# Performance work log

Measured on AMD Instinct MI355X. Metric: run time of the kernel, lower is better.

Reference implementation:

```python
import jax, jax.numpy as jnp
import numpy as np

N_HEADS = 16

def setup_inputs() -> dict:
    key = jax.random.key(0)
    k1, k2, k3 = jax.random.split(key, 3)
    B, S, D = 4, 2048, 1024
    x = jax.random.normal(k1, (B, S, D), dtype=jnp.float32)
    w_in = jax.random.normal(k2, (D, 3 * D), dtype=jnp.float32) * (1.0 / np.sqrt(D))
    b_in = jnp.zeros((3 * D,), dtype=jnp.float32)
    w_out = jax.random.normal(k3, (D, D), dtype=jnp.float32) * (1.0 / np.sqrt(D))
    b_out = jnp.zeros((D,), dtype=jnp.float32)
    return {"x": x, "w_in": w_in, "b_in": b_in, "w_out": w_out, "b_out": b_out}

def reference(x, w_in, b_in, w_out, b_out):
    B, S, D = x.shape
    H = N_HEADS
    dh = D // H
    qkv = x @ w_in + b_in                      # [B,S,3D]
    q, k, v = jnp.split(qkv, 3, axis=-1)
    # [B,S,D] -> [B,H,S,dh]
    q = q.reshape(B, S, H, dh).transpose(0, 2, 1, 3)
    k = k.reshape(B, S, H, dh).transpose(0, 2, 1, 3)
    v = v.reshape(B, S, H, dh).transpose(0, 2, 1, 3)
    scores = jnp.einsum("bhqd,bhkd->bhqk", q, k) / jnp.sqrt(jnp.float32(dh))
    causal = jnp.tril(jnp.ones((S, S), dtype=bool))  # True = keep
    scores = jnp.where(causal, scores, -jnp.inf)
    attn = jax.nn.softmax(scores, axis=-1)
    out = jnp.einsum("bhqk,bhkd->bhqd", attn, v)
    out = out.transpose(0, 2, 1, 3).reshape(B, S, D)
    out = out @ w_out + b_out
    return (out, (k, v))
```

## Files before the change

### kernel.cpp

```cpp
#include <hip/hip_runtime.h>
#include <hip/hip_bf16.h>
#include <math.h>

typedef __bf16 bf16_t;
typedef __bf16 bf16x2 __attribute__((ext_vector_type(2)));
typedef __bf16 bf16x4 __attribute__((ext_vector_type(4)));
typedef __bf16 bf16x8 __attribute__((ext_vector_type(8)));
typedef float floatx4 __attribute__((ext_vector_type(4)));
typedef unsigned short ushort4v __attribute__((ext_vector_type(4)));

#define AS1 __attribute__((address_space(1)))
#define AS3 __attribute__((address_space(3)))

#define BB 4
#define SS 2048
#define DD 1024
#define HH 16
#define DH 64
#define MM (BB * SS)

__device__ __forceinline__ void gld_lds16(const bf16_t* g, bf16_t* l) {
    __builtin_amdgcn_global_load_lds((const AS1 void*)g, (AS3 void*)l, 16, 0, 0);
}

__global__ void detect_dtype(const unsigned short* __restrict__ x, int* __restrict__ flag) {
    if (threadIdx.x == 0) {
        int hits = 0;
        for (int i = 0; i < 128; ++i) {
            int e = (x[i] >> 7) & 0xFF;
            if (e >= 144) ++hits;
        }
        *flag = (hits >= 4) ? 1 : 0;
    }
}

__global__ __launch_bounds__(256)
void convert_x(const void* __restrict__ in, bf16_t* __restrict__ out,
               const int* __restrict__ flag, int n) {
    const int i4 = (blockIdx.x * 256 + threadIdx.x) * 4;
    if (i4 >= n) return;
    if (*flag) {
        floatx4 v = ((const floatx4*)in)[i4 >> 2];
        out[i4 + 0] = (bf16_t)v[0];
        out[i4 + 1] = (bf16_t)v[1];
        out[i4 + 2] = (bf16_t)v[2];
        out[i4 + 3] = (bf16_t)v[3];
    } else {
        ((ushort4v*)out)[i4 >> 2] = ((const ushort4v*)in)[i4 >> 2];
    }
}

__global__ void convert1d(const void* __restrict__ in, bf16_t* __restrict__ out,
                          const int* __restrict__ flag, int n) {
    const int i = blockIdx.x * 256 + threadIdx.x;
    if (i >= n) return;
    out[i] = (*flag) ? (bf16_t)((const float*)in)[i] : ((const bf16_t*)in)[i];
}

__global__ void transpose_cvt(const void* __restrict__ in, bf16_t* __restrict__ out,
                              const int* __restrict__ flag, int R, int C) {
    __shared__ bf16_t tile[32][33];
    const int tx = threadIdx.x & 31;
    const int ty = threadIdx.x >> 5;
    const int r0 = blockIdx.y * 32;
    const int c0 = blockIdx.x * 32;
    if (*flag) {
        const float* fin = (const float*)in;
#pragma unroll
        for (int i = 0; i < 32; i += 8)
            tile[ty + i][tx] = (bf16_t)fin[(size_t)(r0 + ty + i) * C + (c0 + tx)];
    } else {
        const bf16_t* bin = (const bf16_t*)in;
#pragma unroll
        for (int i = 0; i < 32; i += 8)
            tile[ty + i][tx] = bin[(size_t)(r0 + ty + i) * C + (c0 + tx)];
    }
    __syncthreads();
#pragma unroll
    for (int i = 0; i < 32; i += 8)
        out[(size_t)(c0 + ty + i) * R + (r0 + tx)] = tile[tx][ty + i];
}

__global__ __launch_bounds__(256)
void vexpand(const bf16_t* __restrict__ vt, float* __restrict__ vout) {
    __shared__ float tile[32][33];
    const int tx = threadIdx.x & 31;
    const int ty = threadIdx.x >> 5;
    const int s0 = blockIdx.x * 32;
    const int d0 = blockIdx.y * 32;
    const int bh = blockIdx.z;
#pragma unroll
    for (int i = 0; i < 32; i += 8)
        tile[ty + i][tx] = (float)vt[(size_t)(bh * DH + d0 + ty + i) * SS + s0 + tx];
    __syncthreads();
#pragma unroll
    for (int i = 0; i < 32; i += 8)
        vout[((size_t)bh * SS + s0 + ty + i) * DH + d0 + tx] = tile[tx][ty + i];
}

template <int MODE>
__global__ __launch_bounds__(256)
void gemm128(const bf16_t* __restrict__ A, const bf16_t* __restrict__ Bt,
             const bf16_t* __restrict__ bias,
             bf16_t* __restrict__ qout, float* __restrict__ kf,
             bf16_t* __restrict__ kb, bf16_t* __restrict__ vtp,
             float* __restrict__ outf,
             int K, int N) {
    __shared__ bf16_t As[128 * 32];
    __shared__ bf16_t Bs[128 * 32];
    const int tid = threadIdx.x;
    const int wave = tid >> 6;
    const int lane = tid & 63;
    const int quad = lane >> 4;
    const int l16 = lane & 15;
    const int m0 = blockIdx.y * 128;
    const int n0 = blockIdx.x * 128;
    const int wm = (wave & 1) * 64;
    const int wn = (wave >> 1) * 64;

    floatx4 acc[4][4];
#pragma unroll
    for (int i = 0; i < 4; ++i)
#pragma unroll
        for (int j = 0; j < 4; ++j) {
            floatx4 z = {0.f, 0.f, 0.f, 0.f};
            acc[i][j] = z;
        }

    const int srow = wave * 32 + (lane >> 2);
    const int scol = (lane & 3) * 8;
    const bf16_t* ag = A + (size_t)(m0 + srow) * K + scol;
    const bf16_t* bg = Bt + (size_t)(n0 + srow) * K + scol;
    bf16_t* al = As + (wave * 32) * 32;
    bf16_t* bl = Bs + (wave * 32) * 32;

    for (int k0 = 0; k0 < K; k0 += 32) {
        gld_lds16(ag + k0, al);
        gld_lds16(ag + (size_t)16 * K + k0, al + 16 * 32);
        gld_lds16(bg + k0, bl);
        gld_lds16(bg + (size_t)16 * K + k0, bl + 16 * 32);
        __syncthreads();

        bf16x8 af[4], bfv[4];
#pragma unroll
        for (int mt = 0; mt < 4; ++mt)
            af[mt] = *(const bf16x8*)&As[(wm + mt * 16 + l16) * 32 + quad * 8];
#pragma unroll
        for (int nt = 0; nt < 4; ++nt)
            bfv[nt] = *(const bf16x8*)&Bs[(wn + nt * 16 + l16) * 32 + quad * 8];
#pragma unroll
        for (int mt = 0; mt < 4; ++mt)
#pragma unroll
            for (int nt = 0; nt < 4; ++nt)
                acc[mt][nt] = __builtin_amdgcn_mfma_f32_16x16x32_bf16(
                    af[mt], bfv[nt], acc[mt][nt], 0, 0, 0);
        __syncthreads();
    }

#pragma unroll
    for (int mt = 0; mt < 4; ++mt) {
#pragma unroll
        for (int nt = 0; nt < 4; ++nt) {
            const int nc = n0 + wn + nt * 16 + l16;
            const float bv = (float)bias[nc];
            if (MODE == 0) {
                const int sec = nc >> 10;
                const int c = nc & 1023;
                const int h = c >> 6;
                const int dcol = c & 63;
                const int mb = m0 + wm + mt * 16 + quad * 4;
                const int b = mb >> 11;
                const int sbase = mb & 2047;
                if (sec == 2) {
                    bf16x4 pk;
#pragma unroll
                    for (int r = 0; r < 4; ++r) pk[r] = (bf16_t)(acc[mt][nt][r] + bv);
                    *(bf16x4*)&vtp[((size_t)(b * HH + h) * DH + dcol) * SS + sbase] = pk;
                } else {
#pragma unroll
                    for (int r = 0; r < 4; ++r) {
                        const size_t di = ((size_t)(b * HH + h) * SS + sbase + r) * DH + dcol;
                        const float val = acc[mt][nt][r] + bv;
                        if (sec == 0) {
                            qout[di] = (bf16_t)val;
                        } else {
                            kf[di] = val;
                            kb[di] = (bf16_t)val;
                        }
                    }
                }
            } else {
#pragma unroll
                for (int r = 0; r < 4; ++r) {
                    const int m = m0 + wm + mt * 16 + quad * 4 + r;
                    outf[(size_t)m * N + nc] = acc[mt][nt][r] + bv;
                }
            }
        }
    }
}

#define PST 72

__device__ __forceinline__ void stage_kv(const bf16_t* __restrict__ g, int rstride_e,
                                         bf16_t* l, int tid, int wave) {
#pragma unroll
    for (int half = 0; half < 2; ++half) {
        const int row = half * 32 + (tid >> 3);
        const int srcslot = (tid & 7) ^ (row & 7);
        gld_lds16(g + (size_t)row * rstride_e + srcslot * 8,
                  l + half * 2048 + wave * 512);
    }
}

__device__ __forceinline__ bf16x8 ldsfrag(const bf16_t* base, int row, int s) {
    return *(const bf16x8*)&base[row * 64 + ((s ^ (row & 7)) << 3)];
}

__global__ __launch_bounds__(256)
void flash_v5(const bf16_t* __restrict__ q, const bf16_t* __restrict__ kbf,
              const bf16_t* __restrict__ vt, bf16_t* __restrict__ ao) {
    __shared__ bf16_t Ks[2][64 * 64];
    __shared__ bf16_t Vs[64 * 64];
    __shared__ bf16_t Ps[4][16 * PST];
    const int tid = threadIdx.x;
    const int wave = tid >> 6;
    const int lane = tid & 63;
    const int quad = lane >> 4;
    const int l16 = lane & 15;

    const int linear = blockIdx.x;
    const int xcd = linear & 7;
    const int sl = linear >> 3;
    const int hi = sl & 7;
    const int qt = 31 - (sl >> 3);
    const int bh = xcd * 8 + hi;
    const int r0 = qt * 64 + wave * 16;
    const int b = bh >> 4;
    const int h = bh & 15;

    const bf16_t* qp = q + (size_t)bh * SS * DH;
    const bf16_t* kp = kbf + (size_t)bh * SS * DH;
    const bf16_t* vp = vt + (size_t)bh * DH * SS;
    bf16_t* ps = Ps[wave];

    bf16x8 aq0, aq1;
    {
        const bf16_t* qr = qp + (size_t)(r0 + l16) * DH + quad * 8;
        aq0 = *(const bf16x8*)qr;
        aq1 = *(const bf16x8*)(qr + 32);
    }

    floatx4 o[4];
#pragma unroll
    for (int nt = 0; nt < 4; ++nt) {
        floatx4 z = {0.f, 0.f, 0.f, 0.f};
        o[nt] = z;
    }
    float lrow[4] = {0.f, 0.f, 0.f, 0.f};

    const float c2 = 0.18033688011112042f;
    const float FB = 16.0f;
    const int nIter = qt + 1;

    stage_kv(kp, DH, Ks[0], tid, wave);
    asm volatile("s_waitcnt vmcnt(0)" ::: "memory");
    __builtin_amdgcn_s_barrier();

    int cur = 0;
    for (int it = 0; it < nIter; ++it) {
        const int j0 = it * 64;
        stage_kv(vp + j0, SS, Vs, tid, wave);
        if (it + 1 < nIter)
            stage_kv(kp + (size_t)(j0 + 64) * DH, DH, Ks[cur ^ 1], tid, wave);

        const bf16_t* Kc = Ks[cur];
        floatx4 sc[4];
#pragma unroll
        for (int cp = 0; cp < 4; ++cp) {
            const int krow = (cp >> 1) * 32 + 2 * l16 + (cp & 1);
            const bf16x8 kf0 = ldsfrag(Kc, krow, quad);
            const bf16x8 kf1 = ldsfrag(Kc, krow, 4 + quad);
            floatx4 z = {0.f, 0.f, 0.f, 0.f};
            z = __builtin_amdgcn_mfma_f32_16x16x32_bf16(aq0, kf0, z, 0, 0, 0);
            z = __builtin_amdgcn_mfma_f32_16x16x32_bf16(aq1, kf1, z, 0, 0, 0);
            sc[cp] = z;
        }

        if (it == nIter - 1) {
#pragma unroll
            for (int r = 0; r < 4; ++r) {
                const int qi = r0 + quad * 4 + r;
                float p[4];
#pragma unroll
                for (int cp = 0; cp < 4; ++cp) {
                    const int key = j0 + (cp >> 1) * 32 + 2 * l16 + (cp & 1);
                    const float e = __builtin_amdgcn_exp2f(fmaf(sc[cp][r], c2, -FB));
                    p[cp] = (key <= qi) ? e : 0.f;
                }
                lrow[r] += (p[0] + p[1]) + (p[2] + p[3]);
                const int qrow = quad * 4 + r;
                bf16x2 w0, w1;
                w0[0] = (bf16_t)p[0]; w0[1] = (bf16_t)p[1];
                w1[0] = (bf16_t)p[2]; w1[1] = (bf16_t)p[3];
                *(bf16x2*)&ps[qrow * PST + 2 * l16] = w0;
                *(bf16x2*)&ps[qrow * PST + 32 + 2 * l16] = w1;
            }
        } else {
#pragma unroll
            for (int r = 0; r < 4; ++r) {
                float p[4];
#pragma unroll
                for (int cp = 0; cp < 4; ++cp)
                    p[cp] = __builtin_amdgcn_exp2f(fmaf(sc[cp][r], c2, -FB));
                lrow[r] += (p[0] + p[1]) + (p[2] + p[3]);
                const int qrow = quad * 4 + r;
                bf16x2 w0, w1;
                w0[0] = (bf16_t)p[0]; w0[1] = (bf16_t)p[1];
                w1[0] = (bf16_t)p[2]; w1[1] = (bf16_t)p[3];
                *(bf16x2*)&ps[qrow * PST + 2 * l16] = w0;
                *(bf16x2*)&ps[qrow * PST + 32 + 2 * l16] = w1;
            }
        }
        asm volatile("s_waitcnt lgkmcnt(0)" ::: "memory");
        bf16x8 ap0 = *(const bf16x8*)&ps[l16 * PST + quad * 8];
        bf16x8 ap1 = *(const bf16x8*)&ps[l16 * PST + 32 + quad * 8];

        asm volatile("s_waitcnt vmcnt(0) lgkmcnt(0)" ::: "memory");
        __builtin_amdgcn_s_barrier();

#pragma unroll
        for (int nt = 0; nt < 4; ++nt) {
            const int vrow = nt * 16 + l16;
            const bf16x8 vf0 = ldsfrag(Vs, vrow, quad);
            const bf16x8 vf1 = ldsfrag(Vs, vrow, 4 + quad);
            o[nt] = __builtin_amdgcn_mfma_f32_16x16x32_bf16(ap0, vf0, o[nt], 0, 0, 0);
            o[nt] = __builtin_amdgcn_mfma_f32_16x16x32_bf16(ap1, vf1, o[nt], 0, 0, 0);
        }

        asm volatile("s_waitcnt lgkmcnt(0)" ::: "memory");
        __builtin_amdgcn_s_barrier();
        cur ^= 1;
    }

#pragma unroll
    for (int r = 0; r < 4; ++r) {
#pragma unroll
        for (int off = 1; off < 16; off <<= 1)
            lrow[r] += __shfl_xor(lrow[r], off);
    }
#pragma unroll
    for (int r = 0; r < 4; ++r) {
        const float inv = 1.0f / lrow[r];
        const int s = r0 + quad * 4 + r;
        bf16_t* dst = ao + ((size_t)(b * SS + s) * DD) + h * DH;
#pragma unroll
        for (int nt = 0; nt < 4; ++nt)
            dst[nt * 16 + l16] = (bf16_t)(o[nt][r] * inv);
    }
}
#undef PST

extern "C" void kernel_launch(void* const* d_in, const int* in_sizes, int n_in,
                              void* d_out, int out_size, void* d_ws, size_t ws_size,
                              hipStream_t stream) {
    const void* x_raw = nullptr;
    const void* w_in_raw = nullptr;
    const void* b_in_raw = nullptr;
    const void* w_out_raw = nullptr;
    const void* b_out_raw = nullptr;
    for (int i = 0; i < n_in; ++i) {
        switch (in_sizes[i]) {
            case 8388608: x_raw = d_in[i]; break;
            case 3145728: w_in_raw = d_in[i]; break;
            case 3072:    b_in_raw = d_in[i]; break;
            case 1048576: w_out_raw = d_in[i]; break;
            case 1024:    b_out_raw = d_in[i]; break;
            default: break;
        }
    }

    float* outf  = (float*)d_out;
    float* koutf = outf + (size_t)MM * DD;
    float* voutf = koutf + (size_t)MM * DD;

    bf16_t* q_ws = (bf16_t*)d_out;
    bf16_t* k_bf = q_ws + (size_t)MM * DD;

    char* ws = (char*)d_ws;
    int*    flag    = (int*)ws;
    bf16_t* xc      = (bf16_t*)(ws + 256);
    bf16_t* ao_ws   = xc;
    bf16_t* w_in_t  = (bf16_t*)(ws + 16777472);
    bf16_t* w_out_t = (bf16_t*)(ws + 23068928);
    bf16_t* b_in_c  = (bf16_t*)(ws + 25166080);
    bf16_t* b_out_c = (bf16_t*)(ws + 25172224);
    bf16_t* v_t     = (bf16_t*)(ws + 25174272);

    detect_dtype<<<1, 64, 0, stream>>>((const unsigned short*)x_raw, flag);

    convert_x<<<(MM * DD / 4 + 255) / 256, 256, 0, stream>>>(x_raw, xc, flag, MM * DD);
    transpose_cvt<<<dim3(3 * DD / 32, DD / 32), 256, 0, stream>>>(w_in_raw, w_in_t, flag, DD, 3 * DD);
    transpose_cvt<<<dim3(DD / 32, DD / 32), 256, 0, stream>>>(w_out_raw, w_out_t, flag, DD, DD);
    convert1d<<<(3 * DD + 255) / 256, 256, 0, stream>>>(b_in_raw, b_in_c, flag, 3 * DD);
    convert1d<<<(DD + 255) / 256, 256, 0, stream>>>(b_out_raw, b_out_c, flag, DD);

    gemm128<0><<<dim3(3 * DD / 128, MM / 128), 256, 0, stream>>>(
        xc, w_in_t, b_in_c, q_ws, koutf, k_bf, v_t, nullptr, DD, 3 * DD);

    vexpand<<<dim3(SS / 32, DH / 32, BB * HH), 256, 0, stream>>>(v_t, voutf);

    flash_v5<<<dim3((SS / 64) * BB * HH), 256, 0, stream>>>(q_ws, k_bf, v_t, ao_ws);

    gemm128<1><<<dim3(DD / 128, MM / 128), 256, 0, stream>>>(
        ao_ws, w_out_t, b_out_c, nullptr, nullptr, nullptr, nullptr, outf, DD, DD);
}
```

Before: 325.2 us.

## Replace 128x128 GEMM with pipelined 256x256 tile kernel using quad-buffered LDS

Both projection GEMMs now use a 256x256 tile computed by 8 waves, with a 4-slot LDS ring and swizzled layout. Async global-to-LDS loads are interleaved with MFMA phases, paced by explicit vmcnt waits, barriers and setprio. Block indices are remapped to group tiles for L2 locality. The goal is to hide memory latency and raise MFMA utilization over the single-buffered 32-wide K loop. In exchange it hardcodes K=1024, uses much more LDS (128KB per block), and has fewer blocks per GEMM, which may leave CUs underfilled.

Result: no change. 328.7 us (+1.1%).

```diff
diff --git a/kernel.cpp b/kernel.cpp
--- a/kernel.cpp
+++ b/kernel.cpp
@@ -99,104 +99,176 @@
 }
 
 template <int MODE>
-__global__ __launch_bounds__(256)
-void gemm128(const bf16_t* __restrict__ A, const bf16_t* __restrict__ Bt,
+__global__ __launch_bounds__(512, 2)
+void gemm256(const bf16_t* __restrict__ A, const bf16_t* __restrict__ Bt,
              const bf16_t* __restrict__ bias,
              bf16_t* __restrict__ qout, float* __restrict__ kf,
              bf16_t* __restrict__ kb, bf16_t* __restrict__ vtp,
-             float* __restrict__ outf,
-             int K, int N) {
-    __shared__ bf16_t As[128 * 32];
-    __shared__ bf16_t Bs[128 * 32];
+             float* __restrict__ outf, int nbx, int N) {
+    constexpr int KK = 1024;
+    constexpr int NT = KK / 64;
+    __shared__ bf16_t Ah[4][128 * 64];
+    __shared__ bf16_t Bh[4][128 * 64];
     const int tid = threadIdx.x;
-    const int wave = tid >> 6;
-    const int lane = tid & 63;
-    const int quad = lane >> 4;
-    const int l16 = lane & 15;
-    const int m0 = blockIdx.y * 128;
-    const int n0 = blockIdx.x * 128;
-    const int wm = (wave & 1) * 64;
-    const int wn = (wave >> 1) * 64;
-
-    floatx4 acc[4][4];
-#pragma unroll
-    for (int i = 0; i < 4; ++i)
+    const int w = tid >> 6;
+    const int l = tid & 63;
+    const int quad = l >> 4;
+    const int l16 = l & 15;
+    const int wm = w & 1;
+    const int wn = w >> 1;
+
+    const int cpx = gridDim.x >> 3;
+    const int wg = (blockIdx.x & 7) * cpx + (blockIdx.x >> 3);
+    const int m0 = (wg / nbx) * 256;
+    const int n0 = (wg % nbx) * 256;
+
+    const int srow = w * 8 + (l >> 3);
+    const int sg = (l & 7) ^ (srow & 7);
+    const bf16_t* ag = A + (size_t)m0 * KK + (size_t)srow * KK + sg * 8;
+    const bf16_t* bg = Bt + (size_t)n0 * KK + (size_t)srow * KK + sg * 8;
+    const int dst0 = w * 512;
+
+    auto stA = [&](int h) {
+        const bf16_t* g = ag + (size_t)(h & 1) * (128 * KK) + (h >> 1) * 64;
+        bf16_t* s = &Ah[h & 3][dst0];
+        gld_lds16(g, s);
+        gld_lds16(g + (size_t)64 * KK, s + 4096);
+    };
+    auto stB = [&](int h) {
+        const bf16_t* g = bg + (size_t)(h & 1) * (128 * KK) + (h >> 1) * 64;
+        bf16_t* s = &Bh[h & 3][dst0];
+        gld_lds16(g, s);
+        gld_lds16(g + (size_t)64 * KK, s + 4096);
+    };
+
+    const int axor = l16 & 7;
+    auto rdA = [&](int slot, int m, int kh) -> bf16x8 {
+        return *(const bf16x8*)&Ah[slot][(m * 16 + l16) * 64 +
+                                         ((((kh << 2) | quad) ^ axor) << 3)];
+    };
+    auto rdB = [&](int slot, int n, int kh) -> bf16x8 {
+        return *(const bf16x8*)&Bh[slot][((wn & 1) * 64 + n * 16 + l16) * 64 +
+                                         ((((kh << 2) | quad) ^ axor) << 3)];
+    };
+
+    floatx4 acc[8][4];
+#pragma unroll
+    for (int i = 0; i < 8; ++i)
 #pragma unroll
         for (int j = 0; j < 4; ++j) {
             floatx4 z = {0.f, 0.f, 0.f, 0.f};
             acc[i][j] = z;
         }
 
-    const int srow = wave * 32 + (lane >> 2);
-    const int scol = (lane & 3) * 8;
-    const bf16_t* ag = A + (size_t)(m0 + srow) * K + scol;
-    const bf16_t* bg = Bt + (size_t)(n0 + srow) * K + scol;
-    bf16_t* al = As + (wave * 32) * 32;
-    bf16_t* bl = Bs + (wave * 32) * 32;
-
-    for (int k0 = 0; k0 < K; k0 += 32) {
-        gld_lds16(ag + k0, al);
-        gld_lds16(ag + (size_t)16 * K + k0, al + 16 * 32);
-        gld_lds16(bg + k0, bl);
-        gld_lds16(bg + (size_t)16 * K + k0, bl + 16 * 32);
-        __syncthreads();
-
-        bf16x8 af[4], bfv[4];
-#pragma unroll
-        for (int mt = 0; mt < 4; ++mt)
-            af[mt] = *(const bf16x8*)&As[(wm + mt * 16 + l16) * 32 + quad * 8];
-#pragma unroll
-        for (int nt = 0; nt < 4; ++nt)
-            bfv[nt] = *(const bf16x8*)&Bs[(wn + nt * 16 + l16) * 32 + quad * 8];
-#pragma unroll
-        for (int mt = 0; mt < 4; ++mt)
+    stB(0); stB(1); stA(0); stA(1); stB(2); stB(3);
+    asm volatile("s_waitcnt vmcnt(4)" ::: "memory");
+    __builtin_amdgcn_s_barrier();
+
+    bf16x8 bfr[4][2];
+    for (int u = 0; u < NT; ++u) {
+        const int sa = (2 * u + wm) & 3;
+        const int sb = (2 * u + (wn >> 1)) & 3;
+#pragma unroll
+        for (int p = 0; p < 4; ++p) {
+            bf16x8 a00 = rdA(sa, 2 * p, 0),     a01 = rdA(sa, 2 * p, 1);
+            bf16x8 a10 = rdA(sa, 2 * p + 1, 0), a11 = rdA(sa, 2 * p + 1, 1);
+            if (p == 0) {
+#pragma unroll
+                for (int n = 0; n < 4; ++n) {
+                    bfr[n][0] = rdB(sb, n, 0);
+                    bfr[n][1] = rdB(sb, n, 1);
+                }
+            }
+            if (p == 0 && u + 1 < NT) stA(2 * u + 2);
+            if (p == 1 && u + 1 < NT) stA(2 * u + 3);
+            if (p == 2 && u + 2 < NT) stB(2 * u + 4);
+            if (p == 3 && u + 2 < NT) stB(2 * u + 5);
+            if (p == 3 && u + 1 < NT) {
+                if (u + 2 < NT) asm volatile("s_waitcnt vmcnt(4)" ::: "memory");
+                else            asm volatile("s_waitcnt vmcnt(0)" ::: "memory");
+            }
+            __builtin_amdgcn_s_barrier();
+            asm volatile("s_waitcnt lgkmcnt(0)" ::: "memory");
+            __builtin_amdgcn_s_setprio(1);
+#pragma unroll
+            for (int n = 0; n < 4; ++n) {
+                acc[2 * p][n] = __builtin_amdgcn_mfma_f32_16x16x32_bf16(
+                    a00, bfr[n][0], acc[2 * p][n], 0, 0, 0);
+                acc[2 * p][n] = __builtin_amdgcn_mfma_f32_16x16x32_bf16(
+                    a01, bfr[n][1], acc[2 * p][n], 0, 0, 0);
+                acc[2 * p + 1][n] = __builtin_amdgcn_mfma_f32_16x16x32_bf16(
+                    a10, bfr[n][0], acc[2 * p + 1][n], 0, 0, 0);
+                acc[2 * p + 1][n] = __builtin_amdgcn_mfma_f32_16x16x32_bf16(
+                    a11, bfr[n][1], acc[2 * p + 1][n], 0, 0, 0);
+            }
+            __builtin_amdgcn_s_setprio(0);
+            __builtin_amdgcn_s_barrier();
+        }
+    }
+
+    const int nb = n0 + wn * 64;
+    const int mrow0 = m0 + wm * 128;
+    float bv[4];
+#pragma unroll
+    for (int nt = 0; nt < 4; ++nt) bv[nt] = (float)bias[nb + nt * 16 + l16];
+
+    if (MODE == 0) {
+        const int sec = nb >> 10;
+        const int c = nb & 1023;
+        const int hh = c >> 6;
+        const int b = mrow0 >> 11;
+        const int sb0 = mrow0 & 2047;
+        if (sec == 2) {
+#pragma unroll
+            for (int mt = 0; mt < 8; ++mt)
+#pragma unroll
+                for (int nt = 0; nt < 4; ++nt) {
+                    const int dcol = nt * 16 + l16;
+                    const int sbase = sb0 + mt * 16 + quad * 4;
+                    bf16x4 pk;
+#pragma unroll
+                    for (int r = 0; r < 4; ++r) pk[r] = (bf16_t)(acc[mt][nt][r] + bv[nt]);
+                    *(bf16x4*)&vtp[((size_t)(b * HH + hh) * DH + dcol) * SS + sbase] = pk;
+                }
+        } else if (sec == 0) {
+#pragma unroll
+            for (int mt = 0; mt < 8; ++mt)
+#pragma unroll
+                for (int nt = 0; nt < 4; ++nt) {
+                    const int dcol = nt * 16 + l16;
+#pragma unroll
+                    for (int r = 0; r < 4; ++r) {
+                        const int s = sb0 + mt * 16 + quad * 4 + r;
+                        qout[((size_t)(b * HH + hh) * SS + s) * DH + dcol] =
+                            (bf16_t)(acc[mt][nt][r] + bv[nt]);
+                    }
+                }
+        } else {
+#pragma unroll
+            for (int mt = 0; mt < 8; ++mt)
+#pragma unroll
+                for (int nt = 0; nt < 4; ++nt) {
+                    const int dcol = nt * 16 + l16;
+#pragma unroll
+                    for (int r = 0; r < 4; ++r) {
+                        const int s = sb0 + mt * 16 + quad * 4 + r;
+                        const size_t di = ((size_t)(b * HH + hh) * SS + s) * DH + dcol;
+                        const float val = acc[mt][nt][r] + bv[nt];
+                        kf[di] = val;
+                        kb[di] = (bf16_t)val;
+                    }
+                }
+        }
+    } else {
+#pragma unroll
+        for (int mt = 0; mt < 8; ++mt)
 #pragma unroll
             for (int nt = 0; nt < 4; ++nt)
-                acc[mt][nt] = __builtin_amdgcn_mfma_f32_16x16x32_bf16(
-                    af[mt], bfv[nt], acc[mt][nt], 0, 0, 0);
-        __syncthreads();
-    }
-
-#pragma unroll
-    for (int mt = 0; mt < 4; ++mt) {
-#pragma unroll
-        for (int nt = 0; nt < 4; ++nt) {
-            const int nc = n0 + wn + nt * 16 + l16;
-            const float bv = (float)bias[nc];
-            if (MODE == 0) {
-                const int sec = nc >> 10;
-                const int c = nc & 1023;
-                const int h = c >> 6;
-                const int dcol = c & 63;
-                const int mb = m0 + wm + mt * 16 + quad * 4;
-                const int b = mb >> 11;
-                const int sbase = mb & 2047;
-                if (sec == 2) {
-                    bf16x4 pk;
-#pragma unroll
-                    for (int r = 0; r < 4; ++r) pk[r] = (bf16_t)(acc[mt][nt][r] + bv);
-                    *(bf16x4*)&vtp[((size_t)(b * HH + h) * DH + dcol) * SS + sbase] = pk;
-                } else {
-#pragma unroll
-                    for (int r = 0; r < 4; ++r) {
-                        const size_t di = ((size_t)(b * HH + h) * SS + sbase + r) * DH + dcol;
-                        const float val = acc[mt][nt][r] + bv;
-                        if (sec == 0) {
-                            qout[di] = (bf16_t)val;
-                        } else {
-                            kf[di] = val;
-                            kb[di] = (bf16_t)val;
-                        }
-                    }
-                }
-            } else {
 #pragma unroll
                 for (int r = 0; r < 4; ++r) {
-                    const int m = m0 + wm + mt * 16 + quad * 4 + r;
-                    outf[(size_t)m * N + nc] = acc[mt][nt][r] + bv;
-                }
-            }
-        }
+                    const int m = mrow0 + mt * 16 + quad * 4 + r;
+                    outf[(size_t)m * N + nb + nt * 16 + l16] = acc[mt][nt][r] + bv[nt];
+                }
     }
 }
 
@@ -405,13 +477,13 @@
     convert1d<<<(3 * DD + 255) / 256, 256, 0, stream>>>(b_in_raw, b_in_c, flag, 3 * DD);
     convert1d<<<(DD + 255) / 256, 256, 0, stream>>>(b_out_raw, b_out_c, flag, DD);
 
-    gemm128<0><<<dim3(3 * DD / 128, MM / 128), 256, 0, stream>>>(
-        xc, w_in_t, b_in_c, q_ws, koutf, k_bf, v_t, nullptr, DD, 3 * DD);
+    gemm256<0><<<dim3(384), 512, 0, stream>>>(
+        xc, w_in_t, b_in_c, q_ws, koutf, k_bf, v_t, nullptr, 12, 3 * DD);
 
     vexpand<<<dim3(SS / 32, DH / 32, BB * HH), 256, 0, stream>>>(v_t, voutf);
 
     flash_v5<<<dim3((SS / 64) * BB * HH), 256, 0, stream>>>(q_ws, k_bf, v_t, ao_ws);
 
-    gemm128<1><<<dim3(DD / 128, MM / 128), 256, 0, stream>>>(
-        ao_ws, w_out_t, b_out_c, nullptr, nullptr, nullptr, nullptr, outf, DD, DD);
-}
+    gemm256<1><<<dim3(128), 512, 0, stream>>>(
+        ao_ws, w_out_t, b_out_c, nullptr, nullptr, nullptr, nullptr, outf, 4, DD);
+}
```
